# Kernel tuning notes

Measured on AMD Instinct MI355X. Metric: run time of the kernel, lower is better.

## Reference

```python
import jax, jax.numpy as jnp
import numpy as np

N = 50000          # nodes
E = 625000         # edges
H = 128            # hidden_dim
L = 4              # num_layers
G = 2000           # number of graphs in batch
NODE_F = 9
EDGE_F = 4
LN_EPS = 1e-5


def setup_inputs() -> dict:
    key = jax.random.key(0)
    ks = jax.random.split(key, 14)
    s = 0.05
    return {
        "x": jax.random.normal(ks[0], (N, NODE_F), jnp.float32),
        "edge_index": jax.random.randint(ks[1], (2, E), 0, N, dtype=jnp.int32),
        "edge_attr": jax.random.normal(ks[2], (E, EDGE_F), jnp.float32),
        "batch": jnp.sort(jax.random.randint(ks[3], (N,), 0, G, dtype=jnp.int32)),
        # node / edge encoders
        "Wn": jax.random.normal(ks[4], (NODE_F, H), jnp.float32) * s,
        "bn": jnp.zeros((H,), jnp.float32),
        "We": jax.random.normal(ks[5], (EDGE_F, H), jnp.float32) * s,
        "be": jnp.zeros((H,), jnp.float32),
        # per-layer GINE MLP params (stacked over layers)
        "W1": jax.random.normal(ks[6], (L, H, 2 * H), jnp.float32) * s,
        "b1": jnp.zeros((L, 2 * H), jnp.float32),
        "W2": jax.random.normal(ks[7], (L, 2 * H, H), jnp.float32) * s,
        "b2": jnp.zeros((L, H), jnp.float32),
        # per-layer LayerNorm params
        "gamma": jnp.ones((L, H), jnp.float32),
        "beta": jnp.zeros((L, H), jnp.float32),
    }


def reference(x, edge_index, edge_attr, batch, Wn, bn, We, be, W1, b1, W2, b2, gamma, beta):
    h = x @ Wn + bn                       # [N, H]
    ea = edge_attr @ We + be              # [E, H]
    src, dst = edge_index[0], edge_index[1]
    for l in range(L):
        res = h
        # GINEConv (eps=0): out = mlp(x + sum_j relu(x_j + e_ij))
        msg = jax.nn.relu(h[src] + ea)                              # [E, H] gather+add+relu
        agg = jax.ops.segment_sum(msg, dst, num_segments=N)        # scatter-sum -> [N, H]
        z = h + agg
        z = jax.nn.relu(z @ W1[l] + b1[l]) @ W2[l] + b2[l]          # 2-layer MLP
        mu = jnp.mean(z, axis=-1, keepdims=True)
        var = jnp.mean((z - mu) ** 2, axis=-1, keepdims=True)
        z = (z - mu) * jax.lax.rsqrt(var + LN_EPS) * gamma[l] + beta[l]
        h = jax.nn.relu(z) + res                                    # relu + residual
    # global_add_pool
    return jax.ops.segment_sum(h, batch, num_segments=G)            # [G, H]
```

## Files before the change

kernel.cpp:

```cpp
#include <hip/hip_runtime.h>

typedef unsigned short ushort_t;
typedef __attribute__((ext_vector_type(8))) __bf16 bf16x8;
typedef __attribute__((ext_vector_type(4))) float f32x4;

#define HD 128
#define NL 4
#define SCAN_C 2048

__device__ __forceinline__ ushort_t f2bf(float f){
  unsigned u = __builtin_bit_cast(unsigned, f);
  unsigned r = (u + 0x7FFFu + ((u >> 16) & 1u)) >> 16;
  return (ushort_t)r;
}

__device__ __forceinline__ float bf2f(ushort_t u){
  unsigned v = ((unsigned)u) << 16;
  return __builtin_bit_cast(float, v);
}

__device__ __forceinline__ f32x4 mfma16(bf16x8 a, bf16x8 b, f32x4 c){
  return __builtin_amdgcn_mfma_f32_16x16x32_bf16(a, b, c, 0, 0, 0);
}

__global__ void hist_kernel(const int* __restrict__ dst, int* __restrict__ deg, int E){
  int e = blockIdx.x * 256 + threadIdx.x;
  if (e < E) atomicAdd(&deg[dst[e]], 1);
}

__global__ void ghist_kernel(const int* __restrict__ batch, int* __restrict__ gdeg, int N){
  int n = blockIdx.x * 256 + threadIdx.x;
  if (n < N) atomicAdd(&gdeg[batch[n]], 1);
}

__global__ void scan_part(const int* __restrict__ in, int* __restrict__ bsum, int n){
  int b = blockIdx.x, tid = threadIdx.x;
  int base = b * SCAN_C + tid * 8;
  int s = 0;
  if (base + 8 <= n){
    int4 a = *(const int4*)(in + base);
    int4 c = *(const int4*)(in + base + 4);
    s = a.x + a.y + a.z + a.w + c.x + c.y + c.z + c.w;
  } else {
    #pragma unroll
    for (int k = 0; k < 8; ++k) if (base + k < n) s += in[base + k];
  }
  #pragma unroll
  for (int o = 1; o < 64; o <<= 1) s += __shfl_xor(s, o, 64);
  __shared__ int ws[4];
  int lane = tid & 63, wid = tid >> 6;
  if (lane == 0) ws[wid] = s;
  __syncthreads();
  if (tid == 0) bsum[b] = ws[0] + ws[1] + ws[2] + ws[3];
}

__global__ void scan_top(const int* __restrict__ bsum, int* __restrict__ bofs,
                         int* __restrict__ outn, int B){
  int tid = threadIdx.x;
  int v = (tid < B) ? bsum[tid] : 0;
  int lane = tid & 63, wid = tid >> 6;
  int inc = v;
  #pragma unroll
  for (int o = 1; o < 64; o <<= 1){
    int t = __shfl_up(inc, o, 64);
    if (lane >= o) inc += t;
  }
  __shared__ int ws[4];
  if (lane == 63) ws[wid] = inc;
  __syncthreads();
  int wprev = 0;
  for (int i = 0; i < wid; ++i) wprev += ws[i];
  if (tid < B) bofs[tid] = inc - v + wprev;
  if (tid == 0) *outn = ws[0] + ws[1] + ws[2] + ws[3];
}

__global__ void scan_final(const int* __restrict__ in, const int* __restrict__ bofs,
                           int* __restrict__ out, int* __restrict__ cur, int n){
  int b = blockIdx.x, tid = threadIdx.x;
  int base = b * SCAN_C + tid * 8;
  int v[8];
  if (base + 8 <= n){
    *(int4*)(v)     = *(const int4*)(in + base);
    *(int4*)(v + 4) = *(const int4*)(in + base + 4);
  } else {
    #pragma unroll
    for (int k = 0; k < 8; ++k) v[k] = (base + k < n) ? in[base + k] : 0;
  }
  int tsum = 0;
  #pragma unroll
  for (int k = 0; k < 8; ++k) tsum += v[k];
  int lane = tid & 63, wid = tid >> 6;
  int inc = tsum;
  #pragma unroll
  for (int o = 1; o < 64; o <<= 1){
    int t = __shfl_up(inc, o, 64);
    if (lane >= o) inc += t;
  }
  __shared__ int ws[4];
  if (lane == 63) ws[wid] = inc;
  __syncthreads();
  int run = bofs[b] + inc - tsum;
  for (int i = 0; i < wid; ++i) run += ws[i];
  #pragma unroll
  for (int k = 0; k < 8; ++k){
    int i = base + k;
    if (i < n){
      out[i] = run;
      if (cur) cur[i] = run;
      run += v[k];
    }
  }
}

__global__ void scatter_kernel(const int* __restrict__ dst, int* __restrict__ cursor,
                               int* __restrict__ perm, int E){
  int e = blockIdx.x * 256 + threadIdx.x;
  if (e < E){
    int d = dst[e];
    int p = atomicAdd(&cursor[d], 1);
    perm[p] = e;
  }
}

__global__ void permute_kernel(const int* __restrict__ perm, const int* __restrict__ src,
                               const float4* __restrict__ ea, int* __restrict__ srcs_s,
                               float4* __restrict__ ea4p, int E){
  int p = blockIdx.x * 256 + threadIdx.x;
  if (p < E){
    int e = perm[p];
    srcs_s[p] = src[e];
    ea4p[p] = ea[e];
  }
}

__global__ void wconv_kernel(const float* __restrict__ W1, const float* __restrict__ W2,
                             ushort_t* __restrict__ W1t, ushort_t* __restrict__ W2t){
  int i = blockIdx.x * 256 + threadIdx.x;
  if (i < NL * 32768){
    int l = i >> 15, r = i & 32767;
    int n = r >> 7, k = r & 127;
    W1t[i] = f2bf(W1[l * 32768 + k * 256 + n]);
  } else {
    int i2 = i - NL * 32768;
    int l = i2 >> 15, r = i2 & 32767;
    int n = r >> 8, k = r & 255;
    W2t[i2] = f2bf(W2[l * 32768 + k * 128 + n]);
  }
}

__global__ void encoder_kernel(const float* __restrict__ x, const float* __restrict__ Wn,
                               const float* __restrict__ bn, float* __restrict__ h,
                               ushort_t* __restrict__ hb, int N){
  int n = blockIdx.x, j = threadIdx.x;
  float acc = bn[j];
  #pragma unroll
  for (int k = 0; k < 9; ++k) acc = fmaf(x[n * 9 + k], Wn[k * HD + j], acc);
  h[(size_t)n * HD + j] = acc;
  hb[(size_t)n * HD + j] = f2bf(acc);
}

__global__ void agg_kernel(const float* __restrict__ h, const ushort_t* __restrict__ hb,
                           const int* __restrict__ off, const int* __restrict__ srcs,
                           const float4* __restrict__ ea4, const float* __restrict__ We,
                           const float* __restrict__ be, ushort_t* __restrict__ z, int N){
  int n = blockIdx.x, j = threadIdx.x;
  float w0 = We[j], w1 = We[HD + j], w2 = We[2 * HD + j], w3 = We[3 * HD + j];
  float bj = be[j];
  int s = off[n], e = off[n + 1];
  float acc = h[(size_t)n * HD + j];
  int i = s;
  for (; i + 4 <= e; i += 4){
    int s0 = srcs[i], s1 = srcs[i + 1], s2 = srcs[i + 2], s3 = srcs[i + 3];
    float4 a0 = ea4[i], a1 = ea4[i + 1], a2 = ea4[i + 2], a3 = ea4[i + 3];
    float h0 = bf2f(hb[(size_t)s0 * HD + j]);
    float h1 = bf2f(hb[(size_t)s1 * HD + j]);
    float h2 = bf2f(hb[(size_t)s2 * HD + j]);
    float h3 = bf2f(hb[(size_t)s3 * HD + j]);
    float e0 = fmaf(a0.x, w0, fmaf(a0.y, w1, fmaf(a0.z, w2, fmaf(a0.w, w3, bj))));
    float e1 = fmaf(a1.x, w0, fmaf(a1.y, w1, fmaf(a1.z, w2, fmaf(a1.w, w3, bj))));
    float e2 = fmaf(a2.x, w0, fmaf(a2.y, w1, fmaf(a2.z, w2, fmaf(a2.w, w3, bj))));
    float e3 = fmaf(a3.x, w0, fmaf(a3.y, w1, fmaf(a3.z, w2, fmaf(a3.w, w3, bj))));
    acc += fmaxf(h0 + e0, 0.f);
    acc += fmaxf(h1 + e1, 0.f);
    acc += fmaxf(h2 + e2, 0.f);
    acc += fmaxf(h3 + e3, 0.f);
  }
  for (; i < e; ++i){
    int sc = srcs[i];
    float4 a = ea4[i];
    float eav = fmaf(a.x, w0, fmaf(a.y, w1, fmaf(a.z, w2, fmaf(a.w, w3, bj))));
    acc += fmaxf(bf2f(hb[(size_t)sc * HD + j]) + eav, 0.f);
  }
  z[(size_t)n * HD + j] = f2bf(acc);
}

__global__ __launch_bounds__(512, 4) void mlp_fused_kernel(
    const ushort_t* __restrict__ zin, const ushort_t* __restrict__ W1t,
    const float* __restrict__ b1, const ushort_t* __restrict__ W2t,
    const float* __restrict__ b2, const float* __restrict__ gamma,
    const float* __restrict__ beta, float* __restrict__ h,
    ushort_t* __restrict__ hb, int N){
  extern __shared__ char lds[];
  char* tbase = lds + 16384;
  int tid = threadIdx.x;
  int r0 = blockIdx.x * 64;
  #pragma unroll
  for (int i = 0; i < 2; ++i){
    int g = i * 512 + tid;
    int row = g >> 4, kg = g & 15;
    int lb = row * 256 + ((kg * 16) ^ ((row & 7) << 4));
    int ar = min(r0 + row, N - 1);
    *(bf16x8*)(lds + lb) = *(const bf16x8*)(zin + (size_t)ar * 128 + kg * 8);
  }
  int w = tid >> 6, l = tid & 63;
  int lr = l & 15, lk = l >> 4;
  __syncthreads();
  {
    int wk = w >> 1, wn = w & 1;
    f32x4 acc1[4][2] = {};
    #pragma unroll
    for (int ks = 0; ks < 4; ++ks){
      int kb = ks * 64 + lk * 16;
      bf16x8 a[4], b[2];
      #pragma unroll
      for (int fm = 0; fm < 4; ++fm){
        int k2r = wk * 64 + fm * 16 + lr;
        a[fm] = *(const bf16x8*)((const char*)W1t + (size_t)k2r * 256 + kb);
      }
      #pragma unroll
      for (int fn = 0; fn < 2; ++fn){
        int node = wn * 32 + fn * 16 + lr;
        b[fn] = *(const bf16x8*)(lds + node * 256 + (kb ^ ((node & 7) << 4)));
      }
      #pragma unroll
      for (int fm = 0; fm < 4; ++fm)
        #pragma unroll
        for (int fn = 0; fn < 2; ++fn)
          acc1[fm][fn] = mfma16(a[fm], b[fn], acc1[fm][fn]);
    }
    __syncthreads();
    #pragma unroll
    for (int fm = 0; fm < 4; ++fm){
      f32x4 bv = *(const f32x4*)(b1 + wk * 64 + fm * 16 + lk * 4);
      int k2b = (wk * 64 + fm * 16 + lk * 4) * 2;
      #pragma unroll
      for (int fn = 0; fn < 2; ++fn){
        int node = wn * 32 + fn * 16 + lr;
        ushort4 tv;
        tv.x = f2bf(fmaxf(acc1[fm][fn][0] + bv[0], 0.f));
        tv.y = f2bf(fmaxf(acc1[fm][fn][1] + bv[1], 0.f));
        tv.z = f2bf(fmaxf(acc1[fm][fn][2] + bv[2], 0.f));
        tv.w = f2bf(fmaxf(acc1[fm][fn][3] + bv[3], 0.f));
        *(ushort4*)(tbase + node * 512 + (k2b ^ ((node & 7) << 4))) = tv;
      }
    }
  }
  __syncthreads();
  int wd = w >> 1, wn2 = w & 1;
  f32x4 acc2[2][2] = {};
  #pragma unroll
  for (int ks = 0; ks < 8; ++ks){
    int kb = ks * 64 + lk * 16;
    bf16x8 a2[2], bt2[2];
    #pragma unroll
    for (int fm = 0; fm < 2; ++fm){
      int d = wd * 32 + fm * 16 + lr;
      a2[fm] = *(const bf16x8*)((const char*)W2t + (size_t)d * 512 + kb);
    }
    #pragma unroll
    for (int fn = 0; fn < 2; ++fn){
      int node = wn2 * 32 + fn * 16 + lr;
      bt2[fn] = *(const bf16x8*)(tbase + node * 512 + (kb ^ ((node & 7) << 4)));
    }
    #pragma unroll
    for (int fm = 0; fm < 2; ++fm)
      #pragma unroll
      for (int fn = 0; fn < 2; ++fn)
        acc2[fm][fn] = mfma16(a2[fm], bt2[fn], acc2[fm][fn]);
  }
  __syncthreads();
  float* stat_s = (float*)lds;
  float* stat_q = (float*)(lds + 1024);
  f32x4 b2v[2], gv[2], btv[2];
  #pragma unroll
  for (int fm = 0; fm < 2; ++fm){
    int db = wd * 32 + fm * 16 + lk * 4;
    b2v[fm] = *(const f32x4*)(b2 + db);
    gv[fm]  = *(const f32x4*)(gamma + db);
    btv[fm] = *(const f32x4*)(beta + db);
  }
  #pragma unroll
  for (int fn = 0; fn < 2; ++fn){
    float ss = 0.f, qq = 0.f;
    #pragma unroll
    for (int fm = 0; fm < 2; ++fm)
      #pragma unroll
      for (int r = 0; r < 4; ++r){
        float v = acc2[fm][fn][r] + b2v[fm][r];
        acc2[fm][fn][r] = v;
        ss += v; qq += v * v;
      }
    ss += __shfl_xor(ss, 16, 64); ss += __shfl_xor(ss, 32, 64);
    qq += __shfl_xor(qq, 16, 64); qq += __shfl_xor(qq, 32, 64);
    if (l < 16){
      int node = wn2 * 32 + fn * 16 + lr;
      stat_s[node * 4 + wd] = ss;
      stat_q[node * 4 + wd] = qq;
    }
  }
  __syncthreads();
  #pragma unroll
  for (int fn = 0; fn < 2; ++fn){
    int node = wn2 * 32 + fn * 16 + lr;
    int gn = r0 + node;
    float ss = stat_s[node * 4 + 0] + stat_s[node * 4 + 1] +
               stat_s[node * 4 + 2] + stat_s[node * 4 + 3];
    float qq = stat_q[node * 4 + 0] + stat_q[node * 4 + 1] +
               stat_q[node * 4 + 2] + stat_q[node * 4 + 3];
    float mean = ss * (1.f / 128.f);
    float rs = rsqrtf(qq * (1.f / 128.f) - mean * mean + 1e-5f);
    if (gn < N){
      #pragma unroll
      for (int fm = 0; fm < 2; ++fm){
        int db = wd * 32 + fm * 16 + lk * 4;
        f32x4 hold = *(const f32x4*)(h + (size_t)gn * HD + db);
        f32x4 ov;
        #pragma unroll
        for (int r = 0; r < 4; ++r)
          ov[r] = fmaxf((acc2[fm][fn][r] - mean) * rs * gv[fm][r] + btv[fm][r], 0.f) + hold[r];
        *(f32x4*)(h + (size_t)gn * HD + db) = ov;
        ushort4 hv;
        hv.x = f2bf(ov[0]); hv.y = f2bf(ov[1]); hv.z = f2bf(ov[2]); hv.w = f2bf(ov[3]);
        *(ushort4*)(hb + (size_t)gn * HD + db) = hv;
      }
    }
  }
}

__global__ void pool_kernel(const float* __restrict__ h, const int* __restrict__ goff,
                            float* __restrict__ outp, int G){
  int g = blockIdx.x, j = threadIdx.x;
  int s = goff[g], e = goff[g + 1];
  float acc = 0.f;
  for (int i = s; i < e; ++i) acc += h[(size_t)i * HD + j];
  outp[(size_t)g * HD + j] = acc;
}

extern "C" void kernel_launch(void* const* d_in, const int* in_sizes, int n_in,
                              void* d_out, int out_size, void* d_ws, size_t ws_size,
                              hipStream_t stream){
  const float* x     = (const float*)d_in[0];
  const int*   ei    = (const int*)  d_in[1];
  const float* eattr = (const float*)d_in[2];
  const int*   batch = (const int*)  d_in[3];
  const float* Wn    = (const float*)d_in[4];
  const float* bn    = (const float*)d_in[5];
  const float* We    = (const float*)d_in[6];
  const float* be    = (const float*)d_in[7];
  const float* W1    = (const float*)d_in[8];
  const float* b1    = (const float*)d_in[9];
  const float* W2    = (const float*)d_in[10];
  const float* b2    = (const float*)d_in[11];
  const float* gamma = (const float*)d_in[12];
  const float* beta  = (const float*)d_in[13];
  float* outp = (float*)d_out;

  int N = in_sizes[3];
  int E = in_sizes[2] / 4;
  int G = out_size / HD;

  char* base = (char*)d_ws;
  size_t o = 0;
  auto alloc = [&](size_t bytes)->char*{
    char* r = base + o; o = (o + bytes + 255) & ~(size_t)255; return r;
  };
  float*    h    = (float*)   alloc((size_t)N * HD * 4);
  ushort_t* hb   = (ushort_t*)alloc((size_t)N * HD * 2);
  ushort_t* z    = (ushort_t*)alloc((size_t)N * HD * 2);
  ushort_t* W1t  = (ushort_t*)alloc((size_t)NL * 2 * HD * HD * 2);
  ushort_t* W2t  = (ushort_t*)alloc((size_t)NL * 2 * HD * HD * 2);
  int* deg    = (int*)alloc((size_t)N * 4);
  int* gdeg   = (int*)alloc((size_t)G * 4);
  int* off    = (int*)alloc((size_t)(N + 1) * 4);
  int* goff   = (int*)alloc((size_t)(G + 1) * 4);
  int* cursor = (int*)alloc((size_t)N * 4);
  int* bsumN  = (int*)alloc(512 * 4);
  int* bofsN  = (int*)alloc(512 * 4);
  int* bsumG  = (int*)alloc(512 * 4);
  int* bofsG  = (int*)alloc(512 * 4);
  int* perm   = (int*)alloc((size_t)E * 4);
  int* srcs_s = (int*)alloc((size_t)E * 4);
  float4* ea4p= (float4*)alloc((size_t)E * 16);
  (void)ws_size; (void)n_in;

  const int* src = ei;
  const int* dst = ei + E;

  hipMemsetAsync(deg, 0, (size_t)N * 4, stream);
  hipMemsetAsync(gdeg, 0, (size_t)G * 4, stream);

  hist_kernel<<<(E + 255) / 256, 256, 0, stream>>>(dst, deg, E);
  ghist_kernel<<<(N + 255) / 256, 256, 0, stream>>>(batch, gdeg, N);

  int BN = (N + SCAN_C - 1) / SCAN_C;
  int BG = (G + SCAN_C - 1) / SCAN_C;
  scan_part<<<BN, 256, 0, stream>>>(deg, bsumN, N);
  scan_top<<<1, 256, 0, stream>>>(bsumN, bofsN, off + N, BN);
  scan_final<<<BN, 256, 0, stream>>>(deg, bofsN, off, cursor, N);
  scan_part<<<BG, 256, 0, stream>>>(gdeg, bsumG, G);
  scan_top<<<1, 256, 0, stream>>>(bsumG, bofsG, goff + G, BG);
  scan_final<<<BG, 256, 0, stream>>>(gdeg, bofsG, goff, (int*)nullptr, G);

  scatter_kernel<<<(E + 255) / 256, 256, 0, stream>>>(dst, cursor, perm, E);
  permute_kernel<<<(E + 255) / 256, 256, 0, stream>>>(perm, src, (const float4*)eattr,
                                                      srcs_s, ea4p, E);
  wconv_kernel<<<(2 * NL * 32768) / 256, 256, 0, stream>>>(W1, W2, W1t, W2t);
  encoder_kernel<<<N, HD, 0, stream>>>(x, Wn, bn, h, hb, N);

  int mblocks = (N + 63) / 64;
  for (int l = 0; l < NL; ++l){
    agg_kernel<<<N, HD, 0, stream>>>(h, hb, off, srcs_s, ea4p, We, be, z, N);
    mlp_fused_kernel<<<mblocks, 512, 49152, stream>>>(
        z, W1t + (size_t)l * 2 * HD * HD, b1 + l * 2 * HD,
        W2t + (size_t)l * 2 * HD * HD, b2 + l * HD,
        gamma + l * HD, beta + l * HD, h, hb, N);
  }
  pool_kernel<<<G, HD, 0, stream>>>(h, goff, outp, G);
}
```

Baseline: 485.3 us.

## Restructure fused MLP so each wave owns 16 full node rows

Measured after the change: 600.4 us. +23.7%, slower.

```diff
diff --git a/kernel.cpp b/kernel.cpp
--- a/kernel.cpp
+++ b/kernel.cpp
@@ -194,145 +194,91 @@
   z[(size_t)n * HD + j] = f2bf(acc);
 }
 
-__global__ __launch_bounds__(512, 4) void mlp_fused_kernel(
+__global__ __launch_bounds__(256, 3) void mlp_fused_kernel(
     const ushort_t* __restrict__ zin, const ushort_t* __restrict__ W1t,
     const float* __restrict__ b1, const ushort_t* __restrict__ W2t,
     const float* __restrict__ b2, const float* __restrict__ gamma,
     const float* __restrict__ beta, float* __restrict__ h,
     ushort_t* __restrict__ hb, int N){
-  extern __shared__ char lds[];
-  char* tbase = lds + 16384;
+  __shared__ char lds[32768];
   int tid = threadIdx.x;
-  int r0 = blockIdx.x * 64;
-  #pragma unroll
-  for (int i = 0; i < 2; ++i){
-    int g = i * 512 + tid;
-    int row = g >> 4, kg = g & 15;
-    int lb = row * 256 + ((kg * 16) ^ ((row & 7) << 4));
-    int ar = min(r0 + row, N - 1);
-    *(bf16x8*)(lds + lb) = *(const bf16x8*)(zin + (size_t)ar * 128 + kg * 8);
-  }
   int w = tid >> 6, l = tid & 63;
   int lr = l & 15, lk = l >> 4;
-  __syncthreads();
-  {
-    int wk = w >> 1, wn = w & 1;
-    f32x4 acc1[4][2] = {};
-    #pragma unroll
-    for (int ks = 0; ks < 4; ++ks){
-      int kb = ks * 64 + lk * 16;
-      bf16x8 a[4], b[2];
+  char* tstrip = lds + w * 8192;
+  int gn = blockIdx.x * 64 + w * 16 + lr;
+  int zr = min(gn, N - 1);
+  int swz = lr << 4;
+
+  f32x4 acc1[16];
+  #pragma unroll
+  for (int i = 0; i < 16; ++i) acc1[i] = (f32x4){0.f, 0.f, 0.f, 0.f};
+  #pragma unroll
+  for (int ks = 0; ks < 4; ++ks){
+    int kb = ks * 64 + lk * 16;
+    bf16x8 b = *(const bf16x8*)((const char*)zin + (size_t)zr * 256 + kb);
+    #pragma unroll
+    for (int tile = 0; tile < 16; ++tile){
+      bf16x8 a = *(const bf16x8*)((const char*)W1t + (size_t)(tile * 16 + lr) * 256 + kb);
+      acc1[tile] = mfma16(a, b, acc1[tile]);
+    }
+  }
+  #pragma unroll
+  for (int tile = 0; tile < 16; ++tile){
+    f32x4 bv = *(const f32x4*)(b1 + tile * 16 + lk * 4);
+    ushort4 tv;
+    tv.x = f2bf(fmaxf(acc1[tile][0] + bv[0], 0.f));
+    tv.y = f2bf(fmaxf(acc1[tile][1] + bv[1], 0.f));
+    tv.z = f2bf(fmaxf(acc1[tile][2] + bv[2], 0.f));
+    tv.w = f2bf(fmaxf(acc1[tile][3] + bv[3], 0.f));
+    int off = tile * 32 + lk * 8;
+    *(ushort4*)(tstrip + lr * 512 + (off ^ swz)) = tv;
+  }
+
+  f32x4 acc2[8];
+  #pragma unroll
+  for (int i = 0; i < 8; ++i) acc2[i] = (f32x4){0.f, 0.f, 0.f, 0.f};
+  #pragma unroll
+  for (int ks2 = 0; ks2 < 8; ++ks2){
+    int kb2 = ks2 * 64 + lk * 16;
+    bf16x8 bt = *(const bf16x8*)(tstrip + lr * 512 + (kb2 ^ swz));
+    #pragma unroll
+    for (int dt = 0; dt < 8; ++dt){
+      bf16x8 a = *(const bf16x8*)((const char*)W2t + (size_t)(dt * 16 + lr) * 512 + kb2);
+      acc2[dt] = mfma16(a, bt, acc2[dt]);
+    }
+  }
+
+  float ss = 0.f, qq = 0.f;
+  #pragma unroll
+  for (int dt = 0; dt < 8; ++dt){
+    f32x4 bv = *(const f32x4*)(b2 + dt * 16 + lk * 4);
+    #pragma unroll
+    for (int r = 0; r < 4; ++r){
+      float v = acc2[dt][r] + bv[r];
+      acc2[dt][r] = v;
+      ss += v; qq += v * v;
+    }
+  }
+  ss += __shfl_xor(ss, 16, 64); ss += __shfl_xor(ss, 32, 64);
+  qq += __shfl_xor(qq, 16, 64); qq += __shfl_xor(qq, 32, 64);
+  float mean = ss * (1.f / 128.f);
+  float rs = rsqrtf(qq * (1.f / 128.f) - mean * mean + 1e-5f);
+
+  if (gn < N){
+    #pragma unroll
+    for (int dt = 0; dt < 8; ++dt){
+      int db = dt * 16 + lk * 4;
+      f32x4 gv  = *(const f32x4*)(gamma + db);
+      f32x4 btv = *(const f32x4*)(beta + db);
+      f32x4 hold = *(const f32x4*)(h + (size_t)gn * HD + db);
+      f32x4 ov;
       #pragma unroll
-      for (int fm = 0; fm < 4; ++fm){
-        int k2r = wk * 64 + fm * 16 + lr;
-        a[fm] = *(const bf16x8*)((const char*)W1t + (size_t)k2r * 256 + kb);
-      }
-      #pragma unroll
-      for (int fn = 0; fn < 2; ++fn){
-        int node = wn * 32 + fn * 16 + lr;
-        b[fn] = *(const bf16x8*)(lds + node * 256 + (kb ^ ((node & 7) << 4)));
-      }
-      #pragma unroll
-      for (int fm = 0; fm < 4; ++fm)
-        #pragma unroll
-        for (int fn = 0; fn < 2; ++fn)
-          acc1[fm][fn] = mfma16(a[fm], b[fn], acc1[fm][fn]);
-    }
-    __syncthreads();
-    #pragma unroll
-    for (int fm = 0; fm < 4; ++fm){
-      f32x4 bv = *(const f32x4*)(b1 + wk * 64 + fm * 16 + lk * 4);
-      int k2b = (wk * 64 + fm * 16 + lk * 4) * 2;
-      #pragma unroll
-      for (int fn = 0; fn < 2; ++fn){
-        int node = wn * 32 + fn * 16 + lr;
-        ushort4 tv;
-        tv.x = f2bf(fmaxf(acc1[fm][fn][0] + bv[0], 0.f));
-        tv.y = f2bf(fmaxf(acc1[fm][fn][1] + bv[1], 0.f));
-        tv.z = f2bf(fmaxf(acc1[fm][fn][2] + bv[2], 0.f));
-        tv.w = f2bf(fmaxf(acc1[fm][fn][3] + bv[3], 0.f));
-        *(ushort4*)(tbase + node * 512 + (k2b ^ ((node & 7) << 4))) = tv;
-      }
-    }
-  }
-  __syncthreads();
-  int wd = w >> 1, wn2 = w & 1;
-  f32x4 acc2[2][2] = {};
-  #pragma unroll
-  for (int ks = 0; ks < 8; ++ks){
-    int kb = ks * 64 + lk * 16;
-    bf16x8 a2[2], bt2[2];
-    #pragma unroll
-    for (int fm = 0; fm < 2; ++fm){
-      int d = wd * 32 + fm * 16 + lr;
-      a2[fm] = *(const bf16x8*)((const char*)W2t + (size_t)d * 512 + kb);
-    }
-    #pragma unroll
-    for (int fn = 0; fn < 2; ++fn){
-      int node = wn2 * 32 + fn * 16 + lr;
-      bt2[fn] = *(const bf16x8*)(tbase + node * 512 + (kb ^ ((node & 7) << 4)));
-    }
-    #pragma unroll
-    for (int fm = 0; fm < 2; ++fm)
-      #pragma unroll
-      for (int fn = 0; fn < 2; ++fn)
-        acc2[fm][fn] = mfma16(a2[fm], bt2[fn], acc2[fm][fn]);
-  }
-  __syncthreads();
-  float* stat_s = (float*)lds;
-  float* stat_q = (float*)(lds + 1024);
-  f32x4 b2v[2], gv[2], btv[2];
-  #pragma unroll
-  for (int fm = 0; fm < 2; ++fm){
-    int db = wd * 32 + fm * 16 + lk * 4;
-    b2v[fm] = *(const f32x4*)(b2 + db);
-    gv[fm]  = *(const f32x4*)(gamma + db);
-    btv[fm] = *(const f32x4*)(beta + db);
-  }
-  #pragma unroll
-  for (int fn = 0; fn < 2; ++fn){
-    float ss = 0.f, qq = 0.f;
-    #pragma unroll
-    for (int fm = 0; fm < 2; ++fm)
-      #pragma unroll
-      for (int r = 0; r < 4; ++r){
-        float v = acc2[fm][fn][r] + b2v[fm][r];
-        acc2[fm][fn][r] = v;
-        ss += v; qq += v * v;
-      }
-    ss += __shfl_xor(ss, 16, 64); ss += __shfl_xor(ss, 32, 64);
-    qq += __shfl_xor(qq, 16, 64); qq += __shfl_xor(qq, 32, 64);
-    if (l < 16){
-      int node = wn2 * 32 + fn * 16 + lr;
-      stat_s[node * 4 + wd] = ss;
-      stat_q[node * 4 + wd] = qq;
-    }
-  }
-  __syncthreads();
-  #pragma unroll
-  for (int fn = 0; fn < 2; ++fn){
-    int node = wn2 * 32 + fn * 16 + lr;
-    int gn = r0 + node;
-    float ss = stat_s[node * 4 + 0] + stat_s[node * 4 + 1] +
-               stat_s[node * 4 + 2] + stat_s[node * 4 + 3];
-    float qq = stat_q[node * 4 + 0] + stat_q[node * 4 + 1] +
-               stat_q[node * 4 + 2] + stat_q[node * 4 + 3];
-    float mean = ss * (1.f / 128.f);
-    float rs = rsqrtf(qq * (1.f / 128.f) - mean * mean + 1e-5f);
-    if (gn < N){
-      #pragma unroll
-      for (int fm = 0; fm < 2; ++fm){
-        int db = wd * 32 + fm * 16 + lk * 4;
-        f32x4 hold = *(const f32x4*)(h + (size_t)gn * HD + db);
-        f32x4 ov;
-        #pragma unroll
-        for (int r = 0; r < 4; ++r)
-          ov[r] = fmaxf((acc2[fm][fn][r] - mean) * rs * gv[fm][r] + btv[fm][r], 0.f) + hold[r];
-        *(f32x4*)(h + (size_t)gn * HD + db) = ov;
-        ushort4 hv;
-        hv.x = f2bf(ov[0]); hv.y = f2bf(ov[1]); hv.z = f2bf(ov[2]); hv.w = f2bf(ov[3]);
-        *(ushort4*)(hb + (size_t)gn * HD + db) = hv;
-      }
+      for (int r = 0; r < 4; ++r)
+        ov[r] = fmaxf((acc2[dt][r] - mean) * rs * gv[r] + btv[r], 0.f) + hold[r];
+      *(f32x4*)(h + (size_t)gn * HD + db) = ov;
+      ushort4 hv;
+      hv.x = f2bf(ov[0]); hv.y = f2bf(ov[1]); hv.z = f2bf(ov[2]); hv.w = f2bf(ov[3]);
+      *(ushort4*)(hb + (size_t)gn * HD + db) = hv;
     }
   }
 }
@@ -420,7 +366,7 @@
   int mblocks = (N + 63) / 64;
   for (int l = 0; l < NL; ++l){
     agg_kernel<<<N, HD, 0, stream>>>(h, hb, off, srcs_s, ea4p, We, be, z, N);
-    mlp_fused_kernel<<<mblocks, 512, 49152, stream>>>(
+    mlp_fused_kernel<<<mblocks, 256, 0, stream>>>(
         z, W1t + (size_t)l * 2 * HD * HD, b1 + l * 2 * HD,
         W2t + (size_t)l * 2 * HD * HD, b2 + l * HD,
         gamma + l * HD, beta + l * HD, h, hb, N);
```
